# Kernel tuning notes

Measured on AMD Instinct MI355X. Metric: run time of the kernel, lower is better.

Reference implementation:

```python
import jax, jax.numpy as jnp
import numpy as np

N = 10000      # nodes
E = 160000     # edges
B = 16         # graphs in batch
F_NODE = 42
F_EDGE = 12
D = 256        # hidden_dim
H = 4          # heads
C = D // H     # per-head channels = 64
L = 5          # num_layers
NEG_SLOPE = 0.2  # GATConv leaky_relu slope


def layernorm(x, g, b, eps=1e-5):
    mu = jnp.mean(x, axis=-1, keepdims=True)
    var = jnp.var(x, axis=-1, keepdims=True)
    return (x - mu) * jax.lax.rsqrt(var + eps) * g + b


def setup_inputs() -> dict:
    key = jax.random.key(0)
    ks = jax.random.split(key, 20)
    def w(i, shape, scale=0.05):
        return jax.random.normal(ks[i], shape, dtype=jnp.float32) * scale
    return {
        "x": jax.random.normal(ks[0], (N, F_NODE), dtype=jnp.float32),
        "edge_attr": jax.random.normal(ks[1], (E, F_EDGE), dtype=jnp.float32),
        "edge_index": jax.random.randint(ks[2], (2, E), 0, N),
        "batch": jnp.sort(jax.random.randint(ks[3], (N,), 0, B)),
        # node / edge encoders
        "enc_w": w(4, (F_NODE, D)), "enc_b": jnp.zeros((D,), jnp.float32),
        "eenc_w": w(5, (F_EDGE, D)), "eenc_b": jnp.zeros((D,), jnp.float32),
        # stacked GAT layer params [L, ...]
        "gat_w": w(6, (L, D, D)),          # lin_src == lin_dst (shared in PyG for Tensor input)
        "att_src": w(7, (L, H, C)),
        "att_dst": w(8, (L, H, C)),
        "att_edge": w(9, (L, H, C)),
        "gat_ew": w(10, (L, D, D)),        # lin_edge
        "gat_b": jnp.zeros((L, D), jnp.float32),
        "ln_g": jnp.ones((L, D), jnp.float32),
        "ln_b": jnp.zeros((L, D), jnp.float32),
        # attention pooling gate MLP
        "gate_w1": w(11, (D, D)), "gate_b1": jnp.zeros((D,), jnp.float32),
        "gate_w2": w(12, (D, 1)), "gate_b2": jnp.zeros((1,), jnp.float32),
        # MLP readout (mlp_layers=2)
        "ro_w1": w(13, (D, D)), "ro_b1": jnp.zeros((D,), jnp.float32),
        "ro_w2": w(14, (D, D)), "ro_b2": jnp.zeros((D,), jnp.float32),
    }


def reference(x, edge_index, edge_attr, batch, enc_w, enc_b, eenc_w, eenc_b,
              gat_w, att_src, att_dst, att_edge, gat_ew, gat_b, ln_g, ln_b,
              gate_w1, gate_b1, gate_w2, gate_b2, ro_w1, ro_b1, ro_w2, ro_b2):
    src0, dst0 = edge_index[0], edge_index[1]

    # encoders (dropout is identity at eval)
    h = jax.nn.relu(x @ enc_w + enc_b)                      # [N, D]
    e = jax.nn.relu(edge_attr @ eenc_w + eenc_b)            # [E, D]

    # GATConv add_self_loops with fill_value='mean': self-loop edge feature is
    # the mean of incoming edge features per destination node.
    esum = jax.ops.segment_sum(e, dst0, num_segments=N)
    cnt = jax.ops.segment_sum(jnp.ones((E,), e.dtype), dst0, num_segments=N)
    e_self = esum / jnp.maximum(cnt, 1.0)[:, None]
    e_full = jnp.concatenate([e, e_self], axis=0)           # [E+N, D]
    loops = jnp.arange(N)
    src = jnp.concatenate([src0, loops])
    dst = jnp.concatenate([dst0, loops])

    for l in range(L):
        xh = (h @ gat_w[l]).reshape(N, H, C)                # [N, H, C]
        a_s = jnp.einsum('nhc,hc->nh', xh, att_src[l])      # [N, H]
        a_d = jnp.einsum('nhc,hc->nh', xh, att_dst[l])
        eh = (e_full @ gat_ew[l]).reshape(-1, H, C)         # [E+N, H, C]
        a_e = jnp.einsum('ehc,hc->eh', eh, att_edge[l])
        alpha = jax.nn.leaky_relu(a_s[src] + a_d[dst] + a_e, NEG_SLOPE)  # [E+N, H]
        # softmax over incoming edges per destination node (stable)
        m = jax.lax.stop_gradient(jax.ops.segment_max(alpha, dst, num_segments=N))
        ex = jnp.exp(alpha - m[dst])
        den = jax.ops.segment_sum(ex, dst, num_segments=N)
        attn = ex / den[dst]                                # [E+N, H]
        msg = xh[src] * attn[:, :, None]                    # [E+N, H, C]
        out = jax.ops.segment_sum(msg, dst, num_segments=N).reshape(N, D) + gat_b[l]
        out = jax.nn.relu(layernorm(out, ln_g[l], ln_b[l]))
        h = h + out                                         # residual

    # GlobalAttention pooling: softmax(gate_nn(h)) per graph, weighted sum
    gate = (jax.nn.relu(h @ gate_w1 + gate_b1) @ gate_w2 + gate_b2)[:, 0]  # [N]
    gm = jax.lax.stop_gradient(jax.ops.segment_max(gate, batch, num_segments=B))
    ge = jnp.exp(gate - gm[batch])
    gd = jax.ops.segment_sum(ge, batch, num_segments=B)
    wgt = ge / gd[batch]
    g_embed = jax.ops.segment_sum(h * wgt[:, None], batch, num_segments=B)  # [B, D]

    # MLP readout
    return jax.nn.relu(g_embed @ ro_w1 + ro_b1) @ ro_w2 + ro_b2  # [B, D]
```

## Files before the change

### kernel.cpp

```cpp
#include <hip/hip_runtime.h>
#include <math.h>

#define DD 256
#define HH 4
#define CC 64
#define LL 5
#define NEG_SLOPE 0.2f
#define LH 20
#define WCAP 192

typedef __bf16 bf16x8 __attribute__((ext_vector_type(8)));
typedef __bf16 bf16x4 __attribute__((ext_vector_type(4)));
typedef float f32x4 __attribute__((ext_vector_type(4)));

static __device__ __forceinline__ float lrelu(float x) {
    return x > 0.0f ? x : NEG_SLOPE * x;
}

__global__ __launch_bounds__(256) void wproj_kernel(
    const float* __restrict__ gat_ew, const float* __restrict__ att_edge,
    float* __restrict__ wproj) {
    int l = blockIdx.x;
    int k = threadIdx.x;
    const float* W = gat_ew + (size_t)l * DD * DD;
    const float* att = att_edge + l * DD;
    for (int hh = 0; hh < HH; ++hh) {
        float s = 0.f;
        #pragma unroll
        for (int c = 0; c < CC; ++c)
            s += W[k * DD + hh * CC + c] * att[hh * CC + c];
        wproj[k * LH + l * HH + hh] = s;
    }
}

__global__ __launch_bounds__(256) void pack_edge_frags_kernel(
    const float* __restrict__ eenc_w, const float* __restrict__ eenc_b,
    const float* __restrict__ wproj, __bf16* __restrict__ wfe,
    __bf16* __restrict__ wfp) {
    int tid = threadIdx.x;
    for (int idx = tid; idx < 16 * 64; idx += 256) {
        int t = idx >> 6, lane = idx & 63;
        int q = lane >> 4, r15 = lane & 15;
        int col = t * 16 + r15;
        #pragma unroll
        for (int j = 0; j < 8; ++j) {
            int k = q * 8 + j;
            float v = (k < 12) ? eenc_w[k * 256 + col]
                               : (k == 12 ? eenc_b[col] : 0.f);
            wfe[(size_t)idx * 8 + j] = (__bf16)v;
        }
    }
    for (int idx = tid; idx < 16 * 64; idx += 256) {
        int sidx = idx >> 6, lane = idx & 63;
        int s = sidx >> 1, t2 = sidx & 1;
        int q = lane >> 4, r15 = lane & 15;
        int col = t2 * 16 + r15;
        #pragma unroll
        for (int j = 0; j < 8; ++j) {
            int k = s * 32 + q * 8 + j;
            float v = (col < LH) ? wproj[k * LH + col] : 0.f;
            wfp[(size_t)idx * 8 + j] = (__bf16)v;
        }
    }
}

__global__ __launch_bounds__(256) void wswizzle_kernel(
    const float* __restrict__ gat_w, const float* __restrict__ gate_w1,
    __bf16* __restrict__ wf) {
    int b = blockIdx.x;
    int l = b >> 5;
    int rem = b & 31;
    int y = rem >> 3, ks = rem & 7;
    int tid = threadIdx.x;
    int t = tid >> 6, lane = tid & 63;
    int q = lane >> 4, r15 = lane & 15;
    const float* W = (l < 5) ? (gat_w + (size_t)l * DD * DD) : gate_w1;
    size_t obase = (((size_t)b * 4 + t) * 64 + lane) * 8;
    int kbase = ks * 32 + q * 8;
    int col = y * 64 + t * 16 + r15;
    #pragma unroll
    for (int j = 0; j < 8; ++j)
        wf[obase + j] = (__bf16)W[(size_t)(kbase + j) * DD + col];
}

__global__ __launch_bounds__(256) void encoder_kernel(
    const float* __restrict__ x, const float* __restrict__ enc_w,
    const float* __restrict__ enc_b, float* __restrict__ h,
    __bf16* __restrict__ hbf, int N) {
    int n = blockIdx.x;
    int tid = threadIdx.x;
    __shared__ float xs[42];
    if (tid < 42) xs[tid] = x[(size_t)n * 42 + tid];
    __syncthreads();
    float acc = enc_b[tid];
    #pragma unroll
    for (int f = 0; f < 42; ++f) acc += xs[f] * enc_w[f * DD + tid];
    float v = fmaxf(acc, 0.f);
    h[(size_t)n * DD + tid] = v;
    hbf[(size_t)n * DD + tid] = (__bf16)v;
}

__global__ __launch_bounds__(256) void edge_mfma_kernel(
    const float* __restrict__ edge_attr, const __bf16* __restrict__ wfe,
    const __bf16* __restrict__ wfp, float* __restrict__ a_e_all, int E) {
    __shared__ __bf16 sm[4][16][264];
    int tid = threadIdx.x;
    int w = tid >> 6, lane = tid & 63;
    int q = lane >> 4, r15 = lane & 15;
    int eb = blockIdx.x * 64 + w * 16;
    int e = eb + r15;
    int ec = min(e, E - 1);
    bf16x8 a1;
    #pragma unroll
    for (int j = 0; j < 8; ++j) a1[j] = (__bf16)0.f;
    if (q == 0) {
        const float4* p = (const float4*)(edge_attr + (size_t)ec * 12);
        float4 p0 = p[0], p1 = p[1];
        a1[0] = (__bf16)p0.x; a1[1] = (__bf16)p0.y; a1[2] = (__bf16)p0.z; a1[3] = (__bf16)p0.w;
        a1[4] = (__bf16)p1.x; a1[5] = (__bf16)p1.y; a1[6] = (__bf16)p1.z; a1[7] = (__bf16)p1.w;
    } else if (q == 1) {
        float4 p2 = *(const float4*)(edge_attr + (size_t)ec * 12 + 8);
        a1[0] = (__bf16)p2.x; a1[1] = (__bf16)p2.y; a1[2] = (__bf16)p2.z; a1[3] = (__bf16)p2.w;
        a1[4] = (__bf16)1.0f;
    }
    const bf16x8* wfeP = (const bf16x8*)wfe;
    f32x4 zero = (f32x4){0.f, 0.f, 0.f, 0.f};
    #pragma unroll
    for (int t = 0; t < 16; ++t) {
        bf16x8 bfr = wfeP[t * 64 + lane];
        f32x4 c = __builtin_amdgcn_mfma_f32_16x16x32_bf16(a1, bfr, zero, 0, 0, 0);
        int col = t * 16 + r15;
        #pragma unroll
        for (int r = 0; r < 4; ++r)
            sm[w][q * 4 + r][col] = (__bf16)fmaxf(c[r], 0.f);
    }
    const bf16x8* wfpP = (const bf16x8*)wfp;
    f32x4 c2[2];
    c2[0] = zero; c2[1] = zero;
    #pragma unroll
    for (int s = 0; s < 8; ++s) {
        bf16x8 a2 = *(const bf16x8*)&sm[w][r15][s * 32 + q * 8];
        #pragma unroll
        for (int t2 = 0; t2 < 2; ++t2)
            c2[t2] = __builtin_amdgcn_mfma_f32_16x16x32_bf16(
                a2, wfpP[(s * 2 + t2) * 64 + lane], c2[t2], 0, 0, 0);
    }
    #pragma unroll
    for (int t2 = 0; t2 < 2; ++t2) {
        int col = t2 * 16 + r15;
        if (col >= LH) continue;
        #pragma unroll
        for (int r = 0; r < 4; ++r) {
            int e2 = eb + q * 4 + r;
            if (e2 < E) a_e_all[(size_t)e2 * LH + col] = c2[t2][r];
        }
    }
}

__global__ void deg_kernel(const int* __restrict__ dst, int* __restrict__ deg, int E) {
    int e = blockIdx.x * 256 + threadIdx.x;
    if (e < E) atomicAdd(&deg[dst[e]], 1);
}

__global__ void self_ae_kernel(const int* __restrict__ row_ptr,
                               const int* __restrict__ csr_eid,
                               float* __restrict__ a_e_all, int N, int E) {
    int i = blockIdx.x * 256 + threadIdx.x;
    if (i >= N * LH) return;
    int n = i / LH;
    int j = i % LH;
    int rs = row_ptr[n], re = row_ptr[n + 1];
    float s = 0.f;
    for (int k = rs; k < re; ++k)
        s += a_e_all[(size_t)csr_eid[k] * LH + j];
    a_e_all[(size_t)(E + n) * LH + j] = s / (float)max(re - rs, 1);
}

__global__ __launch_bounds__(1024) void scan_kernel(const int* __restrict__ deg,
                                                    int* __restrict__ row_ptr,
                                                    int* __restrict__ cursor, int n) {
    __shared__ int buf[1024];
    __shared__ int carry_s;
    int tid = threadIdx.x;
    if (tid == 0) carry_s = 0;
    __syncthreads();
    for (int base = 0; base < n; base += 1024) {
        int i = base + tid;
        int v = (i < n) ? deg[i] : 0;
        buf[tid] = v;
        __syncthreads();
        for (int off = 1; off < 1024; off <<= 1) {
            int t = (tid >= off) ? buf[tid - off] : 0;
            __syncthreads();
            buf[tid] += t;
            __syncthreads();
        }
        int carry = carry_s;
        if (i < n) {
            int ex = carry + buf[tid] - v;
            row_ptr[i] = ex;
            cursor[i] = ex;
        }
        __syncthreads();
        if (tid == 1023) carry_s = carry + buf[1023];
        __syncthreads();
    }
    if (tid == 0) row_ptr[n] = carry_s;
}

__global__ void scatter_kernel(const int* __restrict__ src, const int* __restrict__ dst,
                               int* __restrict__ cursor, int* __restrict__ csr_src,
                               int* __restrict__ csr_eid, int E) {
    int e = blockIdx.x * 256 + threadIdx.x;
    if (e >= E) return;
    int d = dst[e];
    int pos = atomicAdd(&cursor[d], 1);
    csr_src[pos] = src[e];
    csr_eid[pos] = e;
}

__global__ __launch_bounds__(256) void gemm_mfma_kernel(
    const __bf16* __restrict__ hbf, const __bf16* __restrict__ wf,
    __bf16* __restrict__ xhbf, int M,
    const float* __restrict__ att_src, const float* __restrict__ att_dst,
    float* __restrict__ a_s, float* __restrict__ a_d,
    const float* __restrict__ bias, const float* __restrict__ gate_w2,
    const float* __restrict__ gate_b2, float* __restrict__ gate_out) {
    int tid = threadIdx.x;
    int w = tid >> 6, lane = tid & 63;
    int q = lane >> 4, r15 = lane & 15;
    int m0 = blockIdx.x * 64;
    int y = blockIdx.y;
    int arow = m0 + w * 16 + r15;
    int arowc = min(arow, M - 1);
    const __bf16* ap = hbf + (size_t)arowc * DD + q * 8;
    const bf16x8* bp0 = (const bf16x8*)wf + (size_t)(y * 8) * 4 * 64 + lane;
    f32x4 acc[4];
    #pragma unroll
    for (int t = 0; t < 4; ++t) acc[t] = (f32x4){0.f, 0.f, 0.f, 0.f};
    #pragma unroll
    for (int ks = 0; ks < 8; ++ks) {
        bf16x8 a = *(const bf16x8*)(ap + ks * 32);
        const bf16x8* bp = bp0 + (size_t)ks * 4 * 64;
        #pragma unroll
        for (int t = 0; t < 4; ++t) {
            bf16x8 b = bp[(size_t)t * 64];
            acc[t] = __builtin_amdgcn_mfma_f32_16x16x32_bf16(a, b, acc[t], 0, 0, 0);
        }
    }
    if (xhbf) {
        #pragma unroll
        for (int t = 0; t < 4; ++t) {
            int col = y * 64 + t * 16 + r15;
            #pragma unroll
            for (int r = 0; r < 4; ++r) {
                int rc = m0 + w * 16 + q * 4 + r;
                if (rc < M) xhbf[(size_t)rc * DD + col] = (__bf16)acc[t][r];
            }
        }
    }
    if (att_src) {
        #pragma unroll
        for (int r = 0; r < 4; ++r) {
            float ps = 0.f, pd = 0.f;
            #pragma unroll
            for (int t = 0; t < 4; ++t) {
                int col = y * 64 + t * 16 + r15;
                ps += acc[t][r] * att_src[col];
                pd += acc[t][r] * att_dst[col];
            }
            #pragma unroll
            for (int mask = 1; mask < 16; mask <<= 1) {
                ps += __shfl_xor(ps, mask, 64);
                pd += __shfl_xor(pd, mask, 64);
            }
            int rc = m0 + w * 16 + q * 4 + r;
            if (r15 == 0 && rc < M) {
                a_s[rc * HH + y] = ps;
                a_d[rc * HH + y] = pd;
            }
        }
    }
    if (gate_w2) {
        #pragma unroll
        for (int r = 0; r < 4; ++r) {
            float pg = 0.f;
            #pragma unroll
            for (int t = 0; t < 4; ++t) {
                int col = y * 64 + t * 16 + r15;
                pg += fmaxf(acc[t][r] + bias[col], 0.f) * gate_w2[col];
            }
            #pragma unroll
            for (int mask = 1; mask < 16; mask <<= 1) pg += __shfl_xor(pg, mask, 64);
            int rc = m0 + w * 16 + q * 4 + r;
            if (r15 == 0 && rc < M) {
                float add = pg + (y == 0 ? gate_b2[0] : 0.f);
                atomicAdd(&gate_out[rc], add);
            }
        }
    }
}

__global__ __launch_bounds__(256) void gat_message5_kernel(
    const __bf16* __restrict__ xhbf, const float* __restrict__ a_s,
    const float* __restrict__ a_d, const float* __restrict__ a_e,
    const int* __restrict__ row_ptr, const int* __restrict__ csr_src,
    const int* __restrict__ csr_eid, const float* __restrict__ gat_b,
    const float* __restrict__ ln_g, const float* __restrict__ ln_b,
    float* __restrict__ h, __bf16* __restrict__ hbf, int N, int E) {
    __shared__ float lws[4][WCAP * 4];
    int tid = threadIdx.x;
    int w = tid >> 6, lane = tid & 63;
    int n = blockIdx.x * 4 + w;
    if (n >= N) return;
    int hh = lane >> 4, j = lane & 15;
    int rs = row_ptr[n], re = row_ptr[n + 1];
    int deg = re - rs;
    float adn = a_d[n * HH + hh];
    float al_self = lrelu(a_s[n * HH + hh] + adn + a_e[(size_t)(E + n) * LH + hh]);
    float m = al_self, den = 0.f;
    for (int k = rs + j; k < re; k += 16) {
        int kk = k - rs;
        int s = csr_src[k];
        int eid = csr_eid[k];
        float a = lrelu(a_s[s * HH + hh] + adn + a_e[(size_t)eid * LH + hh]);
        if (kk < WCAP) lws[w][kk * 4 + hh] = a;
        float mn = fmaxf(m, a);
        den = den * __expf(m - mn) + __expf(a - mn);
        m = mn;
    }
    #pragma unroll
    for (int off = 1; off < 16; off <<= 1) {
        float m2 = __shfl_xor(m, off, 64);
        float d2 = __shfl_xor(den, off, 64);
        float mn = fmaxf(m, m2);
        den = den * __expf(m - mn) + d2 * __expf(m2 - mn);
        m = mn;
    }
    den += __expf(al_self - m);
    float inv_den = 1.0f / den;
    int cap = min(deg, WCAP);
    for (int kk = j; kk < cap; kk += 16)
        lws[w][kk * 4 + hh] = __expf(lws[w][kk * 4 + hh] - m) * inv_den;
    float wself = __expf(al_self - m) * inv_den;
    bf16x4 xsb = *((const bf16x4*)(xhbf + (size_t)n * DD) + lane);
    float4 acc;
    acc.x = wself * (float)xsb[0]; acc.y = wself * (float)xsb[1];
    acc.z = wself * (float)xsb[2]; acc.w = wself * (float)xsb[3];
    for (int k = rs; k < re; ++k) {
        int kk = k - rs;
        int s = csr_src[k];
        float wgt;
        if (kk < WCAP) wgt = lws[w][kk * 4 + hh];
        else {
            float a = lrelu(a_s[s * HH + hh] + adn + a_e[(size_t)csr_eid[k] * LH + hh]);
            wgt = __expf(a - m) * inv_den;
        }
        bf16x4 xrb = *((const bf16x4*)(xhbf + (size_t)s * DD) + lane);
        acc.x += wgt * (float)xrb[0]; acc.y += wgt * (float)xrb[1];
        acc.z += wgt * (float)xrb[2]; acc.w += wgt * (float)xrb[3];
    }
    float4 gb = *((const float4*)gat_b + lane);
    float4 val;
    val.x = acc.x + gb.x; val.y = acc.y + gb.y;
    val.z = acc.z + gb.z; val.w = acc.w + gb.w;
    float s1 = val.x + val.y + val.z + val.w;
    float s2 = val.x * val.x + val.y * val.y + val.z * val.z + val.w * val.w;
    #pragma unroll
    for (int off = 1; off < 64; off <<= 1) {
        s1 += __shfl_xor(s1, off, 64);
        s2 += __shfl_xor(s2, off, 64);
    }
    float mu = s1 * (1.0f / DD);
    float var = s2 * (1.0f / DD) - mu * mu;
    float rstd = rsqrtf(var + 1e-5f);
    float4 lg = *((const float4*)ln_g + lane);
    float4 lb = *((const float4*)ln_b + lane);
    float4 nv;
    nv.x = fmaxf((val.x - mu) * rstd * lg.x + lb.x, 0.f);
    nv.y = fmaxf((val.y - mu) * rstd * lg.y + lb.y, 0.f);
    nv.z = fmaxf((val.z - mu) * rstd * lg.z + lb.z, 0.f);
    nv.w = fmaxf((val.w - mu) * rstd * lg.w + lb.w, 0.f);
    float4* hp = (float4*)(h + (size_t)n * DD) + lane;
    float4 hv = *hp;
    hv.x += nv.x; hv.y += nv.y; hv.z += nv.z; hv.w += nv.w;
    *hp = hv;
    bf16x4 hb;
    hb[0] = (__bf16)hv.x; hb[1] = (__bf16)hv.y;
    hb[2] = (__bf16)hv.z; hb[3] = (__bf16)hv.w;
    *((bf16x4*)(hbf + (size_t)n * DD) + lane) = hb;
}

__global__ void bstart_kernel(const int* __restrict__ batch, int* __restrict__ bstart,
                              int N, int B) {
    int b = threadIdx.x;
    if (b > B) return;
    int lo = 0, hi = N;
    while (lo < hi) {
        int mid = (lo + hi) >> 1;
        if (batch[mid] < b) lo = mid + 1; else hi = mid;
    }
    bstart[b] = lo;
}

__global__ __launch_bounds__(256) void gseg_kernel(
    const float* __restrict__ gate, const int* __restrict__ bstart,
    float* __restrict__ gmax, float* __restrict__ gden) {
    int b = blockIdx.x;
    int tid = threadIdx.x;
    int s0 = bstart[b], s1 = bstart[b + 1];
    __shared__ float red[256];
    float m = -1e30f;
    for (int i = s0 + tid; i < s1; i += 256) m = fmaxf(m, gate[i]);
    red[tid] = m;
    __syncthreads();
    for (int off = 128; off; off >>= 1) {
        if (tid < off) red[tid] = fmaxf(red[tid], red[tid + off]);
        __syncthreads();
    }
    float gm = red[0];
    __syncthreads();
    float s = 0.f;
    for (int i = s0 + tid; i < s1; i += 256) s += __expf(gate[i] - gm);
    red[tid] = s;
    __syncthreads();
    for (int off = 128; off; off >>= 1) {
        if (tid < off) red[tid] += red[tid + off];
        __syncthreads();
    }
    if (tid == 0) {
        gmax[b] = gm;
        gden[b] = red[0];
    }
}

#define POOL_CHUNK 32
__global__ __launch_bounds__(256) void pool_scatter_kernel(
    const float* __restrict__ h, const float* __restrict__ gate,
    const float* __restrict__ gmax, const float* __restrict__ gden,
    const int* __restrict__ batch, float* __restrict__ g_embed, int N) {
    int i0 = blockIdx.x * POOL_CHUNK;
    int d = threadIdx.x;
    int iend = min(i0 + POOL_CHUNK, N);
    float acc = 0.f;
    int cur = batch[i0];
    for (int i = i0; i < iend; ++i) {
        int b = batch[i];
        if (b != cur) {
            atomicAdd(&g_embed[cur * DD + d], acc);
            acc = 0.f;
            cur = b;
        }
        float wgt = __expf(gate[i] - gmax[b]) / gden[b];
        acc += wgt * h[(size_t)i * DD + d];
    }
    atomicAdd(&g_embed[cur * DD + d], acc);
}

__global__ __launch_bounds__(256) void readout_kernel(
    const float* __restrict__ g_embed, const float* __restrict__ w1,
    const float* __restrict__ b1, const float* __restrict__ w2,
    const float* __restrict__ b2, float* __restrict__ out) {
    int b = blockIdx.x;
    int tid = threadIdx.x;
    __shared__ float gvec[256];
    __shared__ float hid[256];
    gvec[tid] = g_embed[b * DD + tid];
    __syncthreads();
    float hv = b1[tid];
    for (int k = 0; k < DD; ++k) hv += gvec[k] * w1[k * DD + tid];
    hid[tid] = fmaxf(hv, 0.f);
    __syncthreads();
    float o = b2[tid];
    for (int t = 0; t < DD; ++t) o += hid[t] * w2[t * DD + tid];
    out[b * DD + tid] = o;
}

extern "C" void kernel_launch(void* const* d_in, const int* in_sizes, int n_in,
                              void* d_out, int out_size, void* d_ws, size_t ws_size,
                              hipStream_t stream) {
    const float* x        = (const float*)d_in[0];
    const float* edge_attr= (const float*)d_in[1];
    const int*   edge_idx = (const int*)d_in[2];
    const int*   batch    = (const int*)d_in[3];
    const float* enc_w    = (const float*)d_in[4];
    const float* enc_b    = (const float*)d_in[5];
    const float* eenc_w   = (const float*)d_in[6];
    const float* eenc_b   = (const float*)d_in[7];
    const float* gat_w    = (const float*)d_in[8];
    const float* att_src  = (const float*)d_in[9];
    const float* att_dst  = (const float*)d_in[10];
    const float* att_edge = (const float*)d_in[11];
    const float* gat_ew   = (const float*)d_in[12];
    const float* gat_b    = (const float*)d_in[13];
    const float* ln_g     = (const float*)d_in[14];
    const float* ln_b     = (const float*)d_in[15];
    const float* gate_w1  = (const float*)d_in[16];
    const float* gate_b1  = (const float*)d_in[17];
    const float* gate_w2  = (const float*)d_in[18];
    const float* gate_b2  = (const float*)d_in[19];
    const float* ro_w1    = (const float*)d_in[20];
    const float* ro_b1    = (const float*)d_in[21];
    const float* ro_w2    = (const float*)d_in[22];
    const float* ro_b2    = (const float*)d_in[23];
    float* out = (float*)d_out;

    const int N = in_sizes[0] / 42;
    const int E = in_sizes[1] / 12;
    const int B = out_size / DD;

    char* p = (char*)d_ws;
    auto alloc = [&](size_t bytes) {
        char* r = p;
        p += (bytes + 255) & ~(size_t)255;
        return (void*)r;
    };
    float*  h       = (float*)alloc((size_t)N * DD * 4);
    __bf16* hbf     = (__bf16*)alloc((size_t)N * DD * 2);
    __bf16* xhbf    = (__bf16*)alloc((size_t)N * DD * 2);
    float*  a_s     = (float*)alloc((size_t)N * HH * 4);
    float*  a_d     = (float*)alloc((size_t)N * HH * 4);
    float*  a_e_all = (float*)alloc((size_t)(E + N) * LH * 4);
    float*  wproj   = (float*)alloc((size_t)DD * LH * 4);
    __bf16* wfe     = (__bf16*)alloc((size_t)16 * 64 * 8 * 2);
    __bf16* wfp     = (__bf16*)alloc((size_t)16 * 64 * 8 * 2);
    __bf16* wf      = (__bf16*)alloc((size_t)6 * DD * DD * 2);
    float*  gate    = (float*)alloc((size_t)N * 4);
    float*  g_embed = (float*)alloc((size_t)B * DD * 4);
    float*  gmax    = (float*)alloc((size_t)B * 4);
    float*  gden    = (float*)alloc((size_t)B * 4);
    int* deg        = (int*)alloc((size_t)N * 4);
    int* row_ptr    = (int*)alloc((size_t)(N + 1) * 4);
    int* cursor     = (int*)alloc((size_t)N * 4);
    int* csr_src    = (int*)alloc((size_t)E * 4);
    int* csr_eid    = (int*)alloc((size_t)E * 4);
    int* bstart     = (int*)alloc((size_t)(B + 1) * 4);

    const int* src_arr = edge_idx;
    const int* dst_arr = edge_idx + E;

    hipMemsetAsync(deg, 0, (size_t)N * 4, stream);
    hipMemsetAsync(g_embed, 0, (size_t)B * DD * 4, stream);
    hipMemsetAsync(gate, 0, (size_t)N * 4, stream);

    wproj_kernel<<<LL, 256, 0, stream>>>(gat_ew, att_edge, wproj);
    pack_edge_frags_kernel<<<1, 256, 0, stream>>>(eenc_w, eenc_b, wproj, wfe, wfp);
    wswizzle_kernel<<<192, 256, 0, stream>>>(gat_w, gate_w1, wf);
    encoder_kernel<<<N, 256, 0, stream>>>(x, enc_w, enc_b, h, hbf, N);
    deg_kernel<<<(E + 255) / 256, 256, 0, stream>>>(dst_arr, deg, E);
    scan_kernel<<<1, 1024, 0, stream>>>(deg, row_ptr, cursor, N);
    scatter_kernel<<<(E + 255) / 256, 256, 0, stream>>>(
        src_arr, dst_arr, cursor, csr_src, csr_eid, E);
    edge_mfma_kernel<<<(E + 63) / 64, 256, 0, stream>>>(
        edge_attr, wfe, wfp, a_e_all, E);
    self_ae_kernel<<<(N * LH + 255) / 256, 256, 0, stream>>>(
        row_ptr, csr_eid, a_e_all, N, E);

    dim3 ggrid((N + 63) / 64, 4);
    for (int l = 0; l < LL; ++l) {
        gemm_mfma_kernel<<<ggrid, 256, 0, stream>>>(
            hbf, wf + (size_t)l * DD * DD, xhbf, N,
            att_src + l * DD, att_dst + l * DD, a_s, a_d,
            nullptr, nullptr, nullptr, nullptr);
        gat_message5_kernel<<<(N + 3) / 4, 256, 0, stream>>>(
            xhbf, a_s, a_d, a_e_all + l * HH, row_ptr, csr_src, csr_eid,
            gat_b + l * DD, ln_g + l * DD, ln_b + l * DD, h, hbf, N, E);
    }

    gemm_mfma_kernel<<<ggrid, 256, 0, stream>>>(
        hbf, wf + (size_t)5 * DD * DD, nullptr, N,
        nullptr, nullptr, nullptr, nullptr,
        gate_b1, gate_w2, gate_b2, gate);
    bstart_kernel<<<1, 32, 0, stream>>>(batch, bstart, N, B);
    gseg_kernel<<<B, 256, 0, stream>>>(gate, bstart, gmax, gden);
    pool_scatter_kernel<<<(N + POOL_CHUNK - 1) / POOL_CHUNK, 256, 0, stream>>>(
        h, gate, gmax, gden, batch, g_embed, N);
    readout_kernel<<<B, 256, 0, stream>>>(g_embed, ro_w1, ro_b1, ro_w2, ro_b2, out);
}
```

Measured before the change: 466.0 us.

## Store edge attention terms in CSR order, use wave-shuffle scan, unroll gather

The edge MFMA kernel now writes its per-edge attention logits straight into CSR position order, using a pos array filled by the scatter kernel. This removes the csr_eid indirection from the message and self-loop kernels, so their a_e reads become contiguous. The prefix scan is rebuilt from a shared-memory Hillis-Steele loop with many barriers into a wave-shuffle scan with a small cross-wave step. The aggregation loop is unrolled by two so more gathers are in flight. The cost is scattered writes in the edge kernel, which runs once, in exchange for sequential reads in each of the five layers.

```diff
diff --git a/kernel.cpp b/kernel.cpp
--- a/kernel.cpp
+++ b/kernel.cpp
@@ -102,7 +102,8 @@
 
 __global__ __launch_bounds__(256) void edge_mfma_kernel(
     const float* __restrict__ edge_attr, const __bf16* __restrict__ wfe,
-    const __bf16* __restrict__ wfp, float* __restrict__ a_e_all, int E) {
+    const __bf16* __restrict__ wfp, const int* __restrict__ pos,
+    float* __restrict__ a_e_csr, int E) {
     __shared__ __bf16 sm[4][16][264];
     int tid = threadIdx.x;
     int w = tid >> 6, lane = tid & 63;
@@ -152,7 +153,10 @@
         #pragma unroll
         for (int r = 0; r < 4; ++r) {
             int e2 = eb + q * 4 + r;
-            if (e2 < E) a_e_all[(size_t)e2 * LH + col] = c2[t2][r];
+            if (e2 < E) {
+                int pk = pos[e2];
+                a_e_csr[(size_t)pk * LH + col] = c2[t2][r];
+            }
         }
     }
 }
@@ -163,8 +167,7 @@
 }
 
 __global__ void self_ae_kernel(const int* __restrict__ row_ptr,
-                               const int* __restrict__ csr_eid,
-                               float* __restrict__ a_e_all, int N, int E) {
+                               float* __restrict__ a_e_csr, int N, int E) {
     int i = blockIdx.x * 256 + threadIdx.x;
     if (i >= N * LH) return;
     int n = i / LH;
@@ -172,37 +175,49 @@
     int rs = row_ptr[n], re = row_ptr[n + 1];
     float s = 0.f;
     for (int k = rs; k < re; ++k)
-        s += a_e_all[(size_t)csr_eid[k] * LH + j];
-    a_e_all[(size_t)(E + n) * LH + j] = s / (float)max(re - rs, 1);
+        s += a_e_csr[(size_t)k * LH + j];
+    a_e_csr[(size_t)(E + n) * LH + j] = s / (float)max(re - rs, 1);
 }
 
 __global__ __launch_bounds__(1024) void scan_kernel(const int* __restrict__ deg,
                                                     int* __restrict__ row_ptr,
                                                     int* __restrict__ cursor, int n) {
-    __shared__ int buf[1024];
+    __shared__ int wsum[16];
     __shared__ int carry_s;
     int tid = threadIdx.x;
+    int w = tid >> 6, lane = tid & 63;
     if (tid == 0) carry_s = 0;
     __syncthreads();
     for (int base = 0; base < n; base += 1024) {
         int i = base + tid;
         int v = (i < n) ? deg[i] : 0;
-        buf[tid] = v;
+        int carry = carry_s;
+        int s = v;
+        #pragma unroll
+        for (int off = 1; off < 64; off <<= 1) {
+            int t = __shfl_up(s, off, 64);
+            if (lane >= off) s += t;
+        }
+        if (lane == 63) wsum[w] = s;
         __syncthreads();
-        for (int off = 1; off < 1024; off <<= 1) {
-            int t = (tid >= off) ? buf[tid - off] : 0;
-            __syncthreads();
-            buf[tid] += t;
-            __syncthreads();
-        }
-        int carry = carry_s;
+        if (w == 0 && lane < 16) {
+            int ws = wsum[lane];
+            #pragma unroll
+            for (int off = 1; off < 16; off <<= 1) {
+                int t = __shfl_up(ws, off, 64);
+                if (lane >= off) ws += t;
+            }
+            wsum[lane] = ws;
+        }
+        __syncthreads();
+        int waveoff = (w == 0) ? 0 : wsum[w - 1];
         if (i < n) {
-            int ex = carry + buf[tid] - v;
+            int ex = carry + waveoff + s - v;
             row_ptr[i] = ex;
             cursor[i] = ex;
         }
         __syncthreads();
-        if (tid == 1023) carry_s = carry + buf[1023];
+        if (tid == 0) carry_s = carry + wsum[15];
         __syncthreads();
     }
     if (tid == 0) row_ptr[n] = carry_s;
@@ -210,13 +225,13 @@
 
 __global__ void scatter_kernel(const int* __restrict__ src, const int* __restrict__ dst,
                                int* __restrict__ cursor, int* __restrict__ csr_src,
-                               int* __restrict__ csr_eid, int E) {
+                               int* __restrict__ pos, int E) {
     int e = blockIdx.x * 256 + threadIdx.x;
     if (e >= E) return;
     int d = dst[e];
-    int pos = atomicAdd(&cursor[d], 1);
-    csr_src[pos] = src[e];
-    csr_eid[pos] = e;
+    int pk = atomicAdd(&cursor[d], 1);
+    csr_src[pk] = src[e];
+    pos[e] = pk;
 }
 
 __global__ __launch_bounds__(256) void gemm_mfma_kernel(
@@ -301,11 +316,11 @@
     }
 }
 
-__global__ __launch_bounds__(256) void gat_message5_kernel(
+__global__ __launch_bounds__(256) void gat_message6_kernel(
     const __bf16* __restrict__ xhbf, const float* __restrict__ a_s,
     const float* __restrict__ a_d, const float* __restrict__ a_e,
     const int* __restrict__ row_ptr, const int* __restrict__ csr_src,
-    const int* __restrict__ csr_eid, const float* __restrict__ gat_b,
+    const float* __restrict__ gat_b,
     const float* __restrict__ ln_g, const float* __restrict__ ln_b,
     float* __restrict__ h, __bf16* __restrict__ hbf, int N, int E) {
     __shared__ float lws[4][WCAP * 4];
@@ -322,8 +337,7 @@
     for (int k = rs + j; k < re; k += 16) {
         int kk = k - rs;
         int s = csr_src[k];
-        int eid = csr_eid[k];
-        float a = lrelu(a_s[s * HH + hh] + adn + a_e[(size_t)eid * LH + hh]);
+        float a = lrelu(a_s[s * HH + hh] + adn + a_e[(size_t)k * LH + hh]);
         if (kk < WCAP) lws[w][kk * 4 + hh] = a;
         float mn = fmaxf(m, a);
         den = den * __expf(m - mn) + __expf(a - mn);
@@ -347,18 +361,31 @@
     float4 acc;
     acc.x = wself * (float)xsb[0]; acc.y = wself * (float)xsb[1];
     acc.z = wself * (float)xsb[2]; acc.w = wself * (float)xsb[3];
-    for (int k = rs; k < re; ++k) {
-        int kk = k - rs;
-        int s = csr_src[k];
-        float wgt;
-        if (kk < WCAP) wgt = lws[w][kk * 4 + hh];
-        else {
-            float a = lrelu(a_s[s * HH + hh] + adn + a_e[(size_t)csr_eid[k] * LH + hh]);
-            wgt = __expf(a - m) * inv_den;
-        }
-        bf16x4 xrb = *((const bf16x4*)(xhbf + (size_t)s * DD) + lane);
-        acc.x += wgt * (float)xrb[0]; acc.y += wgt * (float)xrb[1];
-        acc.z += wgt * (float)xrb[2]; acc.w += wgt * (float)xrb[3];
+    int k = rs;
+    for (; k + 1 < re; k += 2) {
+        int kk0 = k - rs, kk1 = kk0 + 1;
+        int s0 = csr_src[k], s1_ = csr_src[k + 1];
+        float w0, w1;
+        if (kk0 < WCAP) w0 = lws[w][kk0 * 4 + hh];
+        else w0 = __expf(lrelu(a_s[s0 * HH + hh] + adn + a_e[(size_t)k * LH + hh]) - m) * inv_den;
+        if (kk1 < WCAP) w1 = lws[w][kk1 * 4 + hh];
+        else w1 = __expf(lrelu(a_s[s1_ * HH + hh] + adn + a_e[(size_t)(k + 1) * LH + hh]) - m) * inv_den;
+        bf16x4 x0 = *((const bf16x4*)(xhbf + (size_t)s0 * DD) + lane);
+        bf16x4 x1 = *((const bf16x4*)(xhbf + (size_t)s1_ * DD) + lane);
+        acc.x += w0 * (float)x0[0] + w1 * (float)x1[0];
+        acc.y += w0 * (float)x0[1] + w1 * (float)x1[1];
+        acc.z += w0 * (float)x0[2] + w1 * (float)x1[2];
+        acc.w += w0 * (float)x0[3] + w1 * (float)x1[3];
+    }
+    if (k < re) {
+        int kk0 = k - rs;
+        int s0 = csr_src[k];
+        float w0;
+        if (kk0 < WCAP) w0 = lws[w][kk0 * 4 + hh];
+        else w0 = __expf(lrelu(a_s[s0 * HH + hh] + adn + a_e[(size_t)k * LH + hh]) - m) * inv_den;
+        bf16x4 x0 = *((const bf16x4*)(xhbf + (size_t)s0 * DD) + lane);
+        acc.x += w0 * (float)x0[0]; acc.y += w0 * (float)x0[1];
+        acc.z += w0 * (float)x0[2]; acc.w += w0 * (float)x0[3];
     }
     float4 gb = *((const float4*)gat_b + lane);
     float4 val;
@@ -520,7 +547,7 @@
     __bf16* xhbf    = (__bf16*)alloc((size_t)N * DD * 2);
     float*  a_s     = (float*)alloc((size_t)N * HH * 4);
     float*  a_d     = (float*)alloc((size_t)N * HH * 4);
-    float*  a_e_all = (float*)alloc((size_t)(E + N) * LH * 4);
+    float*  a_e_csr = (float*)alloc((size_t)(E + N) * LH * 4);
     float*  wproj   = (float*)alloc((size_t)DD * LH * 4);
     __bf16* wfe     = (__bf16*)alloc((size_t)16 * 64 * 8 * 2);
     __bf16* wfp     = (__bf16*)alloc((size_t)16 * 64 * 8 * 2);
@@ -533,7 +560,7 @@
     int* row_ptr    = (int*)alloc((size_t)(N + 1) * 4);
     int* cursor     = (int*)alloc((size_t)N * 4);
     int* csr_src    = (int*)alloc((size_t)E * 4);
-    int* csr_eid    = (int*)alloc((size_t)E * 4);
+    int* pos        = (int*)alloc((size_t)E * 4);
     int* bstart     = (int*)alloc((size_t)(B + 1) * 4);
 
     const int* src_arr = edge_idx;
@@ -550,11 +577,11 @@
     deg_kernel<<<(E + 255) / 256, 256, 0, stream>>>(dst_arr, deg, E);
     scan_kernel<<<1, 1024, 0, stream>>>(deg, row_ptr, cursor, N);
     scatter_kernel<<<(E + 255) / 256, 256, 0, stream>>>(
-        src_arr, dst_arr, cursor, csr_src, csr_eid, E);
+        src_arr, dst_arr, cursor, csr_src, pos, E);
     edge_mfma_kernel<<<(E + 63) / 64, 256, 0, stream>>>(
-        edge_attr, wfe, wfp, a_e_all, E);
+        edge_attr, wfe, wfp, pos, a_e_csr, E);
     self_ae_kernel<<<(N * LH + 255) / 256, 256, 0, stream>>>(
-        row_ptr, csr_eid, a_e_all, N, E);
+        row_ptr, a_e_csr, N, E);
 
     dim3 ggrid((N + 63) / 64, 4);
     for (int l = 0; l < LL; ++l) {
@@ -562,8 +589,8 @@
             hbf, wf + (size_t)l * DD * DD, xhbf, N,
             att_src + l * DD, att_dst + l * DD, a_s, a_d,
             nullptr, nullptr, nullptr, nullptr);
-        gat_message5_kernel<<<(N + 3) / 4, 256, 0, stream>>>(
-            xhbf, a_s, a_d, a_e_all + l * HH, row_ptr, csr_src, csr_eid,
+        gat_message6_kernel<<<(N + 3) / 4, 256, 0, stream>>>(
+            xhbf, a_s, a_d, a_e_csr + l * HH, row_ptr, csr_src,
             gat_b + l * DD, ln_g + l * DD, ln_b + l * DD, h, hbf, N, E);
     }
 
```

New measurement: 438.3 us. 5.9% less time.
